# Kernel tuning notes

Hardware: AMD Instinct MI355X
Metric: run time of the kernel (lower is better)

## Reference

```python
import jax, jax.numpy as jnp
import numpy as np

BATCH, D_IN, D_OUT = 2048, 1024, 4096


def setup_inputs() -> dict:
    key = jax.random.key(0)
    kx, kw = jax.random.split(key)
    x = jax.random.normal(kx, (BATCH, D_IN), dtype=jnp.float32)
    W = jax.random.normal(kw, (D_IN, D_OUT), dtype=jnp.float32)  # nn.Parameter init: N(0,1)
    return {"x": x, "W": W}


def reference(x, W):
    # out[b,o] = -1/2 * sum_i (x[b,i] - W[i,o])^2
    # instead of materializing the [B, O, I] broadcast tensor.
    x_sq = jnp.sum(x * x, axis=1, keepdims=True)          # [B, 1]
    w_sq = jnp.sum(W * W, axis=0, keepdims=True)          # [1, O]
    xw = jnp.matmul(x, W)                                  # [B, O] GEMM
    return -0.5 * (x_sq - 2.0 * xw + w_sq)
```

## Files before the change

### kernel.cpp

```cpp
#include <hip/hip_runtime.h>
#include <stdint.h>

#define BATCH 2048
#define DIN   1024
#define DOUT  4096


__device__ __forceinline__ ushort f2bf(float f) {
    uint32_t u = __float_as_uint(f);
    u += 0x7fffu + ((u >> 16) & 1u);
    return (ushort)(u >> 16);
}

__device__ __forceinline__ void async_copy16(const void* gsrc, void* ldst) {
    __builtin_amdgcn_global_load_lds(
        reinterpret_cast<uint32_t __attribute__((address_space(1)))*>(
            reinterpret_cast<uintptr_t>(gsrc)),
        reinterpret_cast<uint32_t __attribute__((address_space(3)))*>(
            reinterpret_cast<uintptr_t>(ldst)),
        16, 0, 0);
}

typedef __bf16 bf16x8 __attribute__((ext_vector_type(8)));
typedef float  f32x4  __attribute__((ext_vector_type(4)));


__global__ __launch_bounds__(256) void prep_x(const float* __restrict__ x,
                                              ushort* __restrict__ xb,
                                              float* __restrict__ xsq) {
    const int row = blockIdx.x;
    const int t = threadIdx.x;
    const float4 v = *(const float4*)(x + (size_t)row * DIN + t * 4);
    ushort4 pk;
    pk.x = f2bf(v.x); pk.y = f2bf(v.y); pk.z = f2bf(v.z); pk.w = f2bf(v.w);
    *(ushort4*)(xb + (size_t)row * DIN + t * 4) = pk;

    float s = v.x * v.x + v.y * v.y + v.z * v.z + v.w * v.w;
    #pragma unroll
    for (int off = 32; off > 0; off >>= 1) s += __shfl_down(s, off);
    __shared__ float ws[4];
    if ((t & 63) == 0) ws[t >> 6] = s;
    __syncthreads();
    if (t == 0) xsq[row] = ws[0] + ws[1] + ws[2] + ws[3];
}

__global__ __launch_bounds__(256) void prep_w(const float* __restrict__ W,
                                              ushort* __restrict__ wbt,
                                              float* __restrict__ wsq) {
    __shared__ float tile[64][65];
    __shared__ float csum[64];
    const int o0 = blockIdx.x * 64;
    const int i0 = blockIdx.y * 64;
    const int t  = threadIdx.x;
    const int c4 = (t & 15) * 4;
    const int r0 = t >> 4;

    if (t < 64) csum[t] = 0.f;
    __syncthreads();

    float ss0 = 0.f, ss1 = 0.f, ss2 = 0.f, ss3 = 0.f;
    #pragma unroll
    for (int p = 0; p < 4; ++p) {
        const int r = r0 + p * 16;
        const float4 v = *(const float4*)&W[(size_t)(i0 + r) * DOUT + o0 + c4];
        tile[r][c4 + 0] = v.x; tile[r][c4 + 1] = v.y;
        tile[r][c4 + 2] = v.z; tile[r][c4 + 3] = v.w;
        ss0 += v.x * v.x; ss1 += v.y * v.y;
        ss2 += v.z * v.z; ss3 += v.w * v.w;
    }
    atomicAdd(&csum[c4 + 0], ss0);
    atomicAdd(&csum[c4 + 1], ss1);
    atomicAdd(&csum[c4 + 2], ss2);
    atomicAdd(&csum[c4 + 3], ss3);
    __syncthreads();
    if (t < 64) atomicAdd(&wsq[o0 + t], csum[t]);

    #pragma unroll
    for (int p = 0; p < 4; ++p) {
        const int orow = r0 + p * 16;
        ushort4 pk;
        pk.x = f2bf(tile[c4 + 0][orow]);
        pk.y = f2bf(tile[c4 + 1][orow]);
        pk.z = f2bf(tile[c4 + 2][orow]);
        pk.w = f2bf(tile[c4 + 3][orow]);
        *(ushort4*)&wbt[(size_t)(o0 + orow) * DIN + i0 + c4] = pk;
    }
}

#define BM 128
#define BN 128
#define BK 64
#define NT (DIN / BK)

__global__ __launch_bounds__(256, 2) void gemm_bt_epi(
    const ushort* __restrict__ A,
    const ushort* __restrict__ Bt,
    const float* __restrict__ xsq,
    const float* __restrict__ wsq,
    float* __restrict__ out) {
    __shared__ __align__(16) ushort sA[2][BM * BK];
    __shared__ __align__(16) ushort sB[2][BN * BK];

    const int tid  = threadIdx.x;
    const int wv   = tid >> 6;
    const int lane = tid & 63;
    const int wr = wv >> 1, wc = wv & 1;
    const int m0 = blockIdx.y * BM;
    const int n0 = blockIdx.x * BN;

    const int srow = tid >> 3;
    const int scol = (((tid & 7) ^ (srow & 7)) << 3);
    const ushort* ag = A  + (size_t)(m0 + srow) * DIN + scol;
    const ushort* bg = Bt + (size_t)(n0 + srow) * DIN + scol;

    const int fr  = lane & 15;
    const int q4  = lane >> 4;
    const int x7  = lane & 7;
    const int arow = wr * 64 + fr;
    const int brow = wc * 64 + fr;
    const int sl0 = ((q4)     ^ x7) << 3;
    const int sl1 = ((4 + q4) ^ x7) << 3;

    f32x4 acc[4][4] = {};

    auto stage = [&](int b, int kt) {
        ushort* da = &sA[b][0] + wv * 512;
        ushort* db = &sB[b][0] + wv * 512;
        #pragma unroll
        for (int q = 0; q < 4; ++q) {
            async_copy16(ag + (size_t)q * 32 * DIN + kt, da + q * 2048);
            async_copy16(bg + (size_t)q * 32 * DIN + kt, db + q * 2048);
        }
    };

    stage(0, 0);
    __syncthreads();
    int cur = 0;

    for (int t = 0; t < NT; ++t) {
        if (t + 1 < NT) stage(cur ^ 1, (t + 1) * BK);

        const ushort* pa = &sA[cur][0];
        const ushort* pb = &sB[cur][0];
        bf16x8 fa[2][4], fb[2][4];
        #pragma unroll
        for (int i = 0; i < 4; ++i) {
            fa[0][i] = *(const bf16x8*)&pa[(arow + i * 16) * BK + sl0];
            fa[1][i] = *(const bf16x8*)&pa[(arow + i * 16) * BK + sl1];
            fb[0][i] = *(const bf16x8*)&pb[(brow + i * 16) * BK + sl0];
            fb[1][i] = *(const bf16x8*)&pb[(brow + i * 16) * BK + sl1];
        }

        #pragma unroll
        for (int ks = 0; ks < 2; ++ks)
            #pragma unroll
            for (int mi = 0; mi < 4; ++mi)
                #pragma unroll
                for (int ni = 0; ni < 4; ++ni)
                    acc[mi][ni] = __builtin_amdgcn_mfma_f32_16x16x32_bf16(
                        fa[ks][mi], fb[ks][ni], acc[mi][ni], 0, 0, 0);

        __syncthreads();
        cur ^= 1;
    }

    const int er = (lane >> 4) * 4;
    const int ec = lane & 15;
    #pragma unroll
    for (int mi = 0; mi < 4; ++mi) {
        const int row = m0 + wr * 64 + mi * 16 + er;
        #pragma unroll
        for (int ni = 0; ni < 4; ++ni) {
            const int col = n0 + wc * 64 + ni * 16 + ec;
            const float wterm = wsq[col];
            #pragma unroll
            for (int r = 0; r < 4; ++r) {
                out[(size_t)(row + r) * DOUT + col] =
                    acc[mi][ni][r] - 0.5f * (xsq[row + r] + wterm);
            }
        }
    }
}


extern "C" void kernel_launch(void* const* d_in, const int* in_sizes, int n_in,
                              void* d_out, int out_size, void* d_ws, size_t ws_size,
                              hipStream_t stream) {
    const float* x = (const float*)d_in[0];
    const float* W = (const float*)d_in[1];
    float* out = (float*)d_out;

    char* ws = (char*)d_ws;
    ushort* xb  = (ushort*)ws;
    ushort* wbt = (ushort*)(ws + (4u << 20));
    float*  xsq = (float*)(ws + (12u << 20));
    float*  wsq = (float*)(ws + (12u << 20) + (16u << 10));

    hipMemsetAsync(wsq, 0, DOUT * sizeof(float), stream);
    prep_x<<<BATCH, 256, 0, stream>>>(x, xb, xsq);
    prep_w<<<dim3(DOUT / 64, DIN / 64), 256, 0, stream>>>(W, wbt, wsq);
    gemm_bt_epi<<<dim3(DOUT / BN, BATCH / BM), 256, 0, stream>>>(xb, wbt, xsq, wsq, out);
}
```

Measured before the change: 104.9 us.

## Fuse prep kernels, drop memset, deepen GEMM pipeline with XCD-aware tile mapping

Merges the x and W preprocessing kernels into one launch and replaces the atomic column-norm accumulation with per-row-block partial sums, so the memset is no longer needed. The GEMM now reduces those partials in its epilogue. The main loop switches from a double-buffered BK=64 pipeline to a 4-slot BK=32 ring, using explicit vmcnt waits, one barrier per step and raised wave priority around the MFMAs. Block indices are remapped so tiles that share data land on the same XCD. The aim is to cut launch overhead and better overlap global loads with MFMA, at the cost of more barriers and 16 extra loads per column in the epilogue.

New measurement: 109.2 us. +4.0%, slower.

```diff
diff --git a/kernel.cpp b/kernel.cpp
--- a/kernel.cpp
+++ b/kernel.cpp
@@ -24,159 +24,174 @@
 typedef __bf16 bf16x8 __attribute__((ext_vector_type(8)));
 typedef float  f32x4  __attribute__((ext_vector_type(4)));
 
-
-__global__ __launch_bounds__(256) void prep_x(const float* __restrict__ x,
-                                              ushort* __restrict__ xb,
-                                              float* __restrict__ xsq) {
-    const int row = blockIdx.x;
+__global__ __launch_bounds__(256) void prep_fused(
+    const float* __restrict__ x, const float* __restrict__ W,
+    ushort* __restrict__ xb, ushort* __restrict__ wbt,
+    float* __restrict__ xsq, float* __restrict__ wsq_part)
+{
+    __shared__ float smem[64 * 65 + 64];
     const int t = threadIdx.x;
-    const float4 v = *(const float4*)(x + (size_t)row * DIN + t * 4);
-    ushort4 pk;
-    pk.x = f2bf(v.x); pk.y = f2bf(v.y); pk.z = f2bf(v.z); pk.w = f2bf(v.w);
-    *(ushort4*)(xb + (size_t)row * DIN + t * 4) = pk;
-
-    float s = v.x * v.x + v.y * v.y + v.z * v.z + v.w * v.w;
-    #pragma unroll
-    for (int off = 32; off > 0; off >>= 1) s += __shfl_down(s, off);
-    __shared__ float ws[4];
-    if ((t & 63) == 0) ws[t >> 6] = s;
-    __syncthreads();
-    if (t == 0) xsq[row] = ws[0] + ws[1] + ws[2] + ws[3];
-}
-
-__global__ __launch_bounds__(256) void prep_w(const float* __restrict__ W,
-                                              ushort* __restrict__ wbt,
-                                              float* __restrict__ wsq) {
-    __shared__ float tile[64][65];
-    __shared__ float csum[64];
-    const int o0 = blockIdx.x * 64;
-    const int i0 = blockIdx.y * 64;
-    const int t  = threadIdx.x;
-    const int c4 = (t & 15) * 4;
-    const int r0 = t >> 4;
-
-    if (t < 64) csum[t] = 0.f;
-    __syncthreads();
-
-    float ss0 = 0.f, ss1 = 0.f, ss2 = 0.f, ss3 = 0.f;
-    #pragma unroll
-    for (int p = 0; p < 4; ++p) {
-        const int r = r0 + p * 16;
-        const float4 v = *(const float4*)&W[(size_t)(i0 + r) * DOUT + o0 + c4];
-        tile[r][c4 + 0] = v.x; tile[r][c4 + 1] = v.y;
-        tile[r][c4 + 2] = v.z; tile[r][c4 + 3] = v.w;
-        ss0 += v.x * v.x; ss1 += v.y * v.y;
-        ss2 += v.z * v.z; ss3 += v.w * v.w;
-    }
-    atomicAdd(&csum[c4 + 0], ss0);
-    atomicAdd(&csum[c4 + 1], ss1);
-    atomicAdd(&csum[c4 + 2], ss2);
-    atomicAdd(&csum[c4 + 3], ss3);
-    __syncthreads();
-    if (t < 64) atomicAdd(&wsq[o0 + t], csum[t]);
-
-    #pragma unroll
-    for (int p = 0; p < 4; ++p) {
-        const int orow = r0 + p * 16;
+
+    if (blockIdx.x < BATCH) {
+        const int row = blockIdx.x;
+        const float4 v = *(const float4*)(x + (size_t)row * DIN + t * 4);
         ushort4 pk;
-        pk.x = f2bf(tile[c4 + 0][orow]);
-        pk.y = f2bf(tile[c4 + 1][orow]);
-        pk.z = f2bf(tile[c4 + 2][orow]);
-        pk.w = f2bf(tile[c4 + 3][orow]);
-        *(ushort4*)&wbt[(size_t)(o0 + orow) * DIN + i0 + c4] = pk;
+        pk.x = f2bf(v.x); pk.y = f2bf(v.y); pk.z = f2bf(v.z); pk.w = f2bf(v.w);
+        *(ushort4*)(xb + (size_t)row * DIN + t * 4) = pk;
+
+        float s = v.x * v.x + v.y * v.y + v.z * v.z + v.w * v.w;
+        #pragma unroll
+        for (int off = 32; off > 0; off >>= 1) s += __shfl_down(s, off);
+        if ((t & 63) == 0) smem[t >> 6] = s;
+        __syncthreads();
+        if (t == 0) xsq[row] = smem[0] + smem[1] + smem[2] + smem[3];
+    } else {
+        const int wblk = blockIdx.x - BATCH;
+        const int o0 = (wblk & 63) * 64;
+        const int i0 = (wblk >> 6) * 64;
+        float (*tile)[65] = (float(*)[65])smem;
+        float* csum = smem + 64 * 65;
+        const int c4 = (t & 15) * 4;
+        const int r0 = t >> 4;
+
+        if (t < 64) csum[t] = 0.f;
+        __syncthreads();
+
+        float ss0 = 0.f, ss1 = 0.f, ss2 = 0.f, ss3 = 0.f;
+        #pragma unroll
+        for (int p = 0; p < 4; ++p) {
+            const int r = r0 + p * 16;
+            const float4 v = *(const float4*)&W[(size_t)(i0 + r) * DOUT + o0 + c4];
+            tile[r][c4 + 0] = v.x; tile[r][c4 + 1] = v.y;
+            tile[r][c4 + 2] = v.z; tile[r][c4 + 3] = v.w;
+            ss0 += v.x * v.x; ss1 += v.y * v.y;
+            ss2 += v.z * v.z; ss3 += v.w * v.w;
+        }
+        atomicAdd(&csum[c4 + 0], ss0);
+        atomicAdd(&csum[c4 + 1], ss1);
+        atomicAdd(&csum[c4 + 2], ss2);
+        atomicAdd(&csum[c4 + 3], ss3);
+        __syncthreads();
+        if (t < 64) wsq_part[(size_t)(wblk >> 6) * DOUT + o0 + t] = csum[t];
+
+        #pragma unroll
+        for (int p = 0; p < 4; ++p) {
+            const int orow = r0 + p * 16;
+            ushort4 pk;
+            pk.x = f2bf(tile[c4 + 0][orow]);
+            pk.y = f2bf(tile[c4 + 1][orow]);
+            pk.z = f2bf(tile[c4 + 2][orow]);
+            pk.w = f2bf(tile[c4 + 3][orow]);
+            *(ushort4*)&wbt[(size_t)(o0 + orow) * DIN + i0 + c4] = pk;
+        }
     }
 }
 
 #define BM 128
 #define BN 128
-#define BK 64
-#define NT (DIN / BK)
-
-__global__ __launch_bounds__(256, 2) void gemm_bt_epi(
+#define BK 32
+#define NSTEP (DIN / BK)
+
+__global__ __launch_bounds__(256, 2) void gemm_epi(
     const ushort* __restrict__ A,
     const ushort* __restrict__ Bt,
     const float* __restrict__ xsq,
-    const float* __restrict__ wsq,
-    float* __restrict__ out) {
-    __shared__ __align__(16) ushort sA[2][BM * BK];
-    __shared__ __align__(16) ushort sB[2][BN * BK];
+    const float* __restrict__ wsq_part,
+    float* __restrict__ out)
+{
+    __shared__ __align__(16) ushort sA[4][BM * BK];
+    __shared__ __align__(16) ushort sB[4][BN * BK];
 
     const int tid  = threadIdx.x;
     const int wv   = tid >> 6;
     const int lane = tid & 63;
     const int wr = wv >> 1, wc = wv & 1;
-    const int m0 = blockIdx.y * BM;
-    const int n0 = blockIdx.x * BN;
-
-    const int srow = tid >> 3;
-    const int scol = (((tid & 7) ^ (srow & 7)) << 3);
+
+    const int bid = blockIdx.x;
+    const int xcd = bid & 7, loc = bid >> 3;
+    const int bx = (xcd & 3) * 8 + (loc & 7);
+    const int by = (xcd >> 2) * 8 + (loc >> 3);
+    const int m0 = by * BM;
+    const int n0 = bx * BN;
+
+    const int srow = wv * 32 + (lane >> 2);
+    const int scol = (((lane & 3) ^ ((lane >> 3) & 3)) << 3);
     const ushort* ag = A  + (size_t)(m0 + srow) * DIN + scol;
     const ushort* bg = Bt + (size_t)(n0 + srow) * DIN + scol;
 
-    const int fr  = lane & 15;
-    const int q4  = lane >> 4;
-    const int x7  = lane & 7;
+    const int fr   = lane & 15;
+    const int kq   = lane >> 4;
+    const int sw   = (fr >> 1) & 3;
+    const int off8 = ((kq ^ sw) << 3);
     const int arow = wr * 64 + fr;
     const int brow = wc * 64 + fr;
-    const int sl0 = ((q4)     ^ x7) << 3;
-    const int sl1 = ((4 + q4) ^ x7) << 3;
 
     f32x4 acc[4][4] = {};
 
-    auto stage = [&](int b, int kt) {
-        ushort* da = &sA[b][0] + wv * 512;
-        ushort* db = &sB[b][0] + wv * 512;
-        #pragma unroll
-        for (int q = 0; q < 4; ++q) {
-            async_copy16(ag + (size_t)q * 32 * DIN + kt, da + q * 2048);
-            async_copy16(bg + (size_t)q * 32 * DIN + kt, db + q * 2048);
-        }
+    auto stage = [&](int set) {
+        const int sl = set & 3;
+        const int kt = set * BK;
+        ushort* da = &sA[sl][wv * 1024];
+        ushort* db = &sB[sl][wv * 1024];
+        async_copy16(ag + kt,                 da);
+        async_copy16(ag + kt + 16 * DIN,      da + 512);
+        async_copy16(bg + kt,                 db);
+        async_copy16(bg + kt + 16 * DIN,      db + 512);
     };
 
-    stage(0, 0);
-    __syncthreads();
-    int cur = 0;
-
-    for (int t = 0; t < NT; ++t) {
-        if (t + 1 < NT) stage(cur ^ 1, (t + 1) * BK);
-
-        const ushort* pa = &sA[cur][0];
-        const ushort* pb = &sB[cur][0];
-        bf16x8 fa[2][4], fb[2][4];
-        #pragma unroll
-        for (int i = 0; i < 4; ++i) {
-            fa[0][i] = *(const bf16x8*)&pa[(arow + i * 16) * BK + sl0];
-            fa[1][i] = *(const bf16x8*)&pa[(arow + i * 16) * BK + sl1];
-            fb[0][i] = *(const bf16x8*)&pb[(brow + i * 16) * BK + sl0];
-            fb[1][i] = *(const bf16x8*)&pb[(brow + i * 16) * BK + sl1];
-        }
-
-        #pragma unroll
-        for (int ks = 0; ks < 2; ++ks)
-            #pragma unroll
-            for (int mi = 0; mi < 4; ++mi)
-                #pragma unroll
-                for (int ni = 0; ni < 4; ++ni)
-                    acc[mi][ni] = __builtin_amdgcn_mfma_f32_16x16x32_bf16(
-                        fa[ks][mi], fb[ks][ni], acc[mi][ni], 0, 0, 0);
-
-        __syncthreads();
-        cur ^= 1;
-    }
+    stage(0); stage(1); stage(2);
+
+#define K_STEP(s, vm) do {                                                    \
+    asm volatile("s_waitcnt vmcnt(" #vm ")" ::: "memory");                    \
+    __builtin_amdgcn_s_barrier();                                             \
+    asm volatile("" ::: "memory");                                            \
+    if ((s) + 3 < NSTEP) stage((s) + 3);                                      \
+    const ushort* pa_ = &sA[(s) & 3][0];                                      \
+    const ushort* pb_ = &sB[(s) & 3][0];                                      \
+    bf16x8 fa[4], fb[4];                                                      \
+    _Pragma("unroll") for (int i = 0; i < 4; ++i) {                           \
+        fa[i] = *(const bf16x8*)&pa_[(arow + i * 16) * BK + off8];            \
+        fb[i] = *(const bf16x8*)&pb_[(brow + i * 16) * BK + off8];            \
+    }                                                                         \
+    __builtin_amdgcn_s_setprio(1);                                            \
+    _Pragma("unroll") for (int mi = 0; mi < 4; ++mi)                          \
+    _Pragma("unroll") for (int ni = 0; ni < 4; ++ni)                          \
+        acc[mi][ni] = __builtin_amdgcn_mfma_f32_16x16x32_bf16(                \
+            fa[mi], fb[ni], acc[mi][ni], 0, 0, 0);                            \
+    __builtin_amdgcn_s_setprio(0);                                            \
+} while (0)
+
+    #pragma unroll
+    for (int s = 0; s < NSTEP - 4; ++s) K_STEP(s, 8);
+    K_STEP(28, 8);
+    K_STEP(29, 8);
+    K_STEP(30, 4);
+    K_STEP(31, 0);
+#undef K_STEP
 
     const int er = (lane >> 4) * 4;
     const int ec = lane & 15;
+
+    float wt[4];
+    #pragma unroll
+    for (int ni = 0; ni < 4; ++ni) {
+        const int col = n0 + wc * 64 + ni * 16 + ec;
+        float s = 0.f;
+        #pragma unroll
+        for (int j = 0; j < 16; ++j) s += wsq_part[(size_t)j * DOUT + col];
+        wt[ni] = s;
+    }
+
     #pragma unroll
     for (int mi = 0; mi < 4; ++mi) {
         const int row = m0 + wr * 64 + mi * 16 + er;
         #pragma unroll
         for (int ni = 0; ni < 4; ++ni) {
             const int col = n0 + wc * 64 + ni * 16 + ec;
-            const float wterm = wsq[col];
             #pragma unroll
             for (int r = 0; r < 4; ++r) {
                 out[(size_t)(row + r) * DOUT + col] =
-                    acc[mi][ni][r] - 0.5f * (xsq[row + r] + wterm);
+                    acc[mi][ni][r] - 0.5f * (xsq[row + r] + wt[ni]);
             }
         }
     }
@@ -194,10 +209,10 @@
     ushort* xb  = (ushort*)ws;
     ushort* wbt = (ushort*)(ws + (4u << 20));
     float*  xsq = (float*)(ws + (12u << 20));
-    float*  wsq = (float*)(ws + (12u << 20) + (16u << 10));
-
-    hipMemsetAsync(wsq, 0, DOUT * sizeof(float), stream);
-    prep_x<<<BATCH, 256, 0, stream>>>(x, xb, xsq);
-    prep_w<<<dim3(DOUT / 64, DIN / 64), 256, 0, stream>>>(W, wbt, wsq);
-    gemm_bt_epi<<<dim3(DOUT / BN, BATCH / BM), 256, 0, stream>>>(xb, wbt, xsq, wsq, out);
-}
+    float*  wsq_part = (float*)(ws + (12u << 20) + (16u << 10));
+
+    prep_fused<<<BATCH + (DOUT / 64) * (DIN / 64), 256, 0, stream>>>(
+        x, W, xb, wbt, xsq, wsq_part);
+    gemm_epi<<<(DOUT / BN) * (BATCH / BM), 256, 0, stream>>>(
+        xb, wbt, xsq, wsq_part, out);
+}
```

## Fuse prep kernels, drop memset via partial sums, remap GEMM blocks, set MFMA priority

Applied to the files above, without the earlier changes.

The x and W preprocessing kernels become one launch that branches on block index. The global atomic accumulation of column norms, and the memset it needed, is replaced by per-k-block partial sums that the GEMM epilogue adds up. The GEMM grid is flattened and remapped so that groups of 8x8 neighbouring tiles run together, which should improve L2 reuse. The MFMA loop is also wrapped in s_setprio raises. These changes cut launch overhead and atomics, at the cost of 16 extra loads per column in the epilogue.

After: 105.0 us. No clear change (+0.1%).

```diff
diff --git a/kernel.cpp b/kernel.cpp
--- a/kernel.cpp
+++ b/kernel.cpp
@@ -24,66 +24,66 @@
 typedef __bf16 bf16x8 __attribute__((ext_vector_type(8)));
 typedef float  f32x4  __attribute__((ext_vector_type(4)));
 
-
-__global__ __launch_bounds__(256) void prep_x(const float* __restrict__ x,
-                                              ushort* __restrict__ xb,
-                                              float* __restrict__ xsq) {
-    const int row = blockIdx.x;
+__global__ __launch_bounds__(256) void prep_fused(
+    const float* __restrict__ x, const float* __restrict__ W,
+    ushort* __restrict__ xb, ushort* __restrict__ wbt,
+    float* __restrict__ xsq, float* __restrict__ wsq_part)
+{
+    __shared__ float smem[64 * 65 + 64];
     const int t = threadIdx.x;
-    const float4 v = *(const float4*)(x + (size_t)row * DIN + t * 4);
-    ushort4 pk;
-    pk.x = f2bf(v.x); pk.y = f2bf(v.y); pk.z = f2bf(v.z); pk.w = f2bf(v.w);
-    *(ushort4*)(xb + (size_t)row * DIN + t * 4) = pk;
-
-    float s = v.x * v.x + v.y * v.y + v.z * v.z + v.w * v.w;
-    #pragma unroll
-    for (int off = 32; off > 0; off >>= 1) s += __shfl_down(s, off);
-    __shared__ float ws[4];
-    if ((t & 63) == 0) ws[t >> 6] = s;
-    __syncthreads();
-    if (t == 0) xsq[row] = ws[0] + ws[1] + ws[2] + ws[3];
-}
-
-__global__ __launch_bounds__(256) void prep_w(const float* __restrict__ W,
-                                              ushort* __restrict__ wbt,
-                                              float* __restrict__ wsq) {
-    __shared__ float tile[64][65];
-    __shared__ float csum[64];
-    const int o0 = blockIdx.x * 64;
-    const int i0 = blockIdx.y * 64;
-    const int t  = threadIdx.x;
-    const int c4 = (t & 15) * 4;
-    const int r0 = t >> 4;
-
-    if (t < 64) csum[t] = 0.f;
-    __syncthreads();
-
-    float ss0 = 0.f, ss1 = 0.f, ss2 = 0.f, ss3 = 0.f;
-    #pragma unroll
-    for (int p = 0; p < 4; ++p) {
-        const int r = r0 + p * 16;
-        const float4 v = *(const float4*)&W[(size_t)(i0 + r) * DOUT + o0 + c4];
-        tile[r][c4 + 0] = v.x; tile[r][c4 + 1] = v.y;
-        tile[r][c4 + 2] = v.z; tile[r][c4 + 3] = v.w;
-        ss0 += v.x * v.x; ss1 += v.y * v.y;
-        ss2 += v.z * v.z; ss3 += v.w * v.w;
-    }
-    atomicAdd(&csum[c4 + 0], ss0);
-    atomicAdd(&csum[c4 + 1], ss1);
-    atomicAdd(&csum[c4 + 2], ss2);
-    atomicAdd(&csum[c4 + 3], ss3);
-    __syncthreads();
-    if (t < 64) atomicAdd(&wsq[o0 + t], csum[t]);
-
-    #pragma unroll
-    for (int p = 0; p < 4; ++p) {
-        const int orow = r0 + p * 16;
+
+    if (blockIdx.x < BATCH) {
+        const int row = blockIdx.x;
+        const float4 v = *(const float4*)(x + (size_t)row * DIN + t * 4);
         ushort4 pk;
-        pk.x = f2bf(tile[c4 + 0][orow]);
-        pk.y = f2bf(tile[c4 + 1][orow]);
-        pk.z = f2bf(tile[c4 + 2][orow]);
-        pk.w = f2bf(tile[c4 + 3][orow]);
-        *(ushort4*)&wbt[(size_t)(o0 + orow) * DIN + i0 + c4] = pk;
+        pk.x = f2bf(v.x); pk.y = f2bf(v.y); pk.z = f2bf(v.z); pk.w = f2bf(v.w);
+        *(ushort4*)(xb + (size_t)row * DIN + t * 4) = pk;
+
+        float s = v.x * v.x + v.y * v.y + v.z * v.z + v.w * v.w;
+        #pragma unroll
+        for (int off = 32; off > 0; off >>= 1) s += __shfl_down(s, off);
+        if ((t & 63) == 0) smem[t >> 6] = s;
+        __syncthreads();
+        if (t == 0) xsq[row] = smem[0] + smem[1] + smem[2] + smem[3];
+    } else {
+        const int wblk = blockIdx.x - BATCH;
+        const int o0 = (wblk & 63) * 64;
+        const int i0 = (wblk >> 6) * 64;
+        float (*tile)[65] = (float(*)[65])smem;
+        float* csum = smem + 64 * 65;
+        const int c4 = (t & 15) * 4;
+        const int r0 = t >> 4;
+
+        if (t < 64) csum[t] = 0.f;
+        __syncthreads();
+
+        float ss0 = 0.f, ss1 = 0.f, ss2 = 0.f, ss3 = 0.f;
+        #pragma unroll
+        for (int p = 0; p < 4; ++p) {
+            const int r = r0 + p * 16;
+            const float4 v = *(const float4*)&W[(size_t)(i0 + r) * DOUT + o0 + c4];
+            tile[r][c4 + 0] = v.x; tile[r][c4 + 1] = v.y;
+            tile[r][c4 + 2] = v.z; tile[r][c4 + 3] = v.w;
+            ss0 += v.x * v.x; ss1 += v.y * v.y;
+            ss2 += v.z * v.z; ss3 += v.w * v.w;
+        }
+        atomicAdd(&csum[c4 + 0], ss0);
+        atomicAdd(&csum[c4 + 1], ss1);
+        atomicAdd(&csum[c4 + 2], ss2);
+        atomicAdd(&csum[c4 + 3], ss3);
+        __syncthreads();
+        if (t < 64) wsq_part[(size_t)(wblk >> 6) * DOUT + o0 + t] = csum[t];
+
+        #pragma unroll
+        for (int p = 0; p < 4; ++p) {
+            const int orow = r0 + p * 16;
+            ushort4 pk;
+            pk.x = f2bf(tile[c4 + 0][orow]);
+            pk.y = f2bf(tile[c4 + 1][orow]);
+            pk.z = f2bf(tile[c4 + 2][orow]);
+            pk.w = f2bf(tile[c4 + 3][orow]);
+            *(ushort4*)&wbt[(size_t)(o0 + orow) * DIN + i0 + c4] = pk;
+        }
     }
 }
 
@@ -92,12 +92,13 @@
 #define BK 64
 #define NT (DIN / BK)
 
-__global__ __launch_bounds__(256, 2) void gemm_bt_epi(
+__global__ __launch_bounds__(256, 2) void gemm_epi(
     const ushort* __restrict__ A,
     const ushort* __restrict__ Bt,
     const float* __restrict__ xsq,
-    const float* __restrict__ wsq,
-    float* __restrict__ out) {
+    const float* __restrict__ wsq_part,
+    float* __restrict__ out)
+{
     __shared__ __align__(16) ushort sA[2][BM * BK];
     __shared__ __align__(16) ushort sB[2][BN * BK];
 
@@ -105,8 +106,13 @@
     const int wv   = tid >> 6;
     const int lane = tid & 63;
     const int wr = wv >> 1, wc = wv & 1;
-    const int m0 = blockIdx.y * BM;
-    const int n0 = blockIdx.x * BN;
+
+    const int bid = blockIdx.x;
+    const int k = bid & 7, loc = bid >> 3;
+    const int bx = (k & 3) * 8 + (loc & 7);
+    const int by = (k >> 2) * 8 + (loc >> 3);
+    const int m0 = by * BM;
+    const int n0 = bx * BN;
 
     const int srow = tid >> 3;
     const int scol = (((tid & 7) ^ (srow & 7)) << 3);
@@ -151,6 +157,7 @@
             fb[1][i] = *(const bf16x8*)&pb[(brow + i * 16) * BK + sl1];
         }
 
+        __builtin_amdgcn_s_setprio(1);
         #pragma unroll
         for (int ks = 0; ks < 2; ++ks)
             #pragma unroll
@@ -159,24 +166,35 @@
                 for (int ni = 0; ni < 4; ++ni)
                     acc[mi][ni] = __builtin_amdgcn_mfma_f32_16x16x32_bf16(
                         fa[ks][mi], fb[ks][ni], acc[mi][ni], 0, 0, 0);
+        __builtin_amdgcn_s_setprio(0);
 
         __syncthreads();
         cur ^= 1;
     }
 
-    const int er = (lane >> 4) * 4;
-    const int ec = lane & 15;
+    const int er = q4 * 4;
+    const int ec = fr;
+
+    float wt[4];
+    #pragma unroll
+    for (int ni = 0; ni < 4; ++ni) {
+        const int col = n0 + wc * 64 + ni * 16 + ec;
+        float s = 0.f;
+        #pragma unroll
+        for (int j = 0; j < 16; ++j) s += wsq_part[(size_t)j * DOUT + col];
+        wt[ni] = s;
+    }
+
     #pragma unroll
     for (int mi = 0; mi < 4; ++mi) {
         const int row = m0 + wr * 64 + mi * 16 + er;
         #pragma unroll
         for (int ni = 0; ni < 4; ++ni) {
             const int col = n0 + wc * 64 + ni * 16 + ec;
-            const float wterm = wsq[col];
             #pragma unroll
             for (int r = 0; r < 4; ++r) {
                 out[(size_t)(row + r) * DOUT + col] =
-                    acc[mi][ni][r] - 0.5f * (xsq[row + r] + wterm);
+                    acc[mi][ni][r] - 0.5f * (xsq[row + r] + wt[ni]);
             }
         }
     }
@@ -194,10 +212,10 @@
     ushort* xb  = (ushort*)ws;
     ushort* wbt = (ushort*)(ws + (4u << 20));
     float*  xsq = (float*)(ws + (12u << 20));
-    float*  wsq = (float*)(ws + (12u << 20) + (16u << 10));
-
-    hipMemsetAsync(wsq, 0, DOUT * sizeof(float), stream);
-    prep_x<<<BATCH, 256, 0, stream>>>(x, xb, xsq);
-    prep_w<<<dim3(DOUT / 64, DIN / 64), 256, 0, stream>>>(W, wbt, wsq);
-    gemm_bt_epi<<<dim3(DOUT / BN, BATCH / BM), 256, 0, stream>>>(xb, wbt, xsq, wsq, out);
-}
+    float*  wsq_part = (float*)(ws + (12u << 20) + (16u << 10));
+
+    prep_fused<<<BATCH + (DOUT / 64) * (DIN / 64), 256, 0, stream>>>(
+        x, W, xb, wbt, xsq, wsq_part);
+    gemm_epi<<<(DOUT / BN) * (BATCH / BM), 256, 0, stream>>>(
+        xb, wbt, xsq, wsq_part, out);
+}
```
